# Optimization experiments

Hardware: AMD Instinct MI355X
Metric: run time of the kernel (lower is better)

Reference implementation:

```python
import jax, jax.numpy as jnp
import numpy as np

WS = 16          # window_size
NUM_HEADS = 6

def _rel_tables(ws):
    # SwinV2 continuous relative coords table, log-spaced, scaled by 8
    r = np.arange(-(ws - 1), ws, dtype=np.float32)
    t = np.stack(np.meshgrid(r, r, indexing='ij'), axis=-1)      # (2ws-1, 2ws-1, 2)
    t = t / (ws - 1) * 8.0
    t = np.sign(t) * np.log2(np.abs(t) + 1.0) / np.log2(8.0)
    c = np.stack(np.meshgrid(np.arange(ws), np.arange(ws), indexing='ij')).reshape(2, -1)
    rel = (c[:, :, None] - c[:, None, :]).transpose(1, 2, 0)     # (N, N, 2)
    rel[..., 0] += ws - 1
    rel[..., 1] += ws - 1
    rel[..., 0] *= 2 * ws - 1
    return jnp.asarray(t), jnp.asarray(rel.sum(-1))              # table, (N,N) int index

REL_TABLE, REL_INDEX = _rel_tables(WS)

def conv2d(x, w, b, pad=0, dil=1, groups=1):
    y = jax.lax.conv_general_dilated(
        x, w, (1, 1), [(pad, pad), (pad, pad)], rhs_dilation=(dil, dil),
        feature_group_count=groups, dimension_numbers=('NCHW', 'OIHW', 'NCHW'))
    return y + b[None, :, None, None]

def layernorm(x, g, b, eps=1e-5):
    mu = x.mean(-1, keepdims=True)
    var = ((x - mu) ** 2).mean(-1, keepdims=True)
    return (x - mu) * jax.lax.rsqrt(var + eps) * g + b

def _forward(x, p1_w, p1_b, pw_w, pw_b, dw_w, dw_b, dd_w, dd_b, p2_w, p2_b,
             ln_g, ln_b, qkv_w, q_bias, v_bias, logit_scale,
             cpb_w1, cpb_b1, cpb_w2, proj_w, proj_b):
    B, C, H, W = x.shape
    ws, nh = WS, NUM_HEADS
    N, hd = ws * ws, C // nh
    # ---- VAB: conv attention block ----
    y = jax.nn.gelu(conv2d(x, p1_w, p1_b), approximate=False)          # proj_1 + GELU
    a = conv2d(y, pw_w, pw_b)                                          # pointwise 1x1
    a = conv2d(a, dw_w, dw_b, pad=2, groups=C)                         # depthwise 5x5
    a = conv2d(a, dd_w, dd_b, pad=6, dil=3, groups=C)                  # depthwise 5x5 dil=3
    y = conv2d(y * a, p2_w, p2_b) + x                                  # proj_2 + residual
    y = jnp.transpose(y, (0, 2, 3, 1))                                 # B,H,W,C
    y = layernorm(y, ln_g, ln_b)                                       # pixel_norm
    # ---- window partition -> (B*nW, N, C) ----
    xw = y.reshape(B, H // ws, ws, W // ws, ws, C)
    xw = xw.transpose(0, 1, 3, 2, 4, 5).reshape(-1, N, C)
    # ---- SwinV2 cosine window attention ----
    qkv_b = jnp.concatenate([q_bias, jnp.zeros_like(v_bias), v_bias])
    qkv = (xw @ qkv_w.T + qkv_b).reshape(-1, N, 3, nh, hd).transpose(2, 0, 3, 1, 4)
    q, k, v = qkv[0], qkv[1], qkv[2]                                   # (B_, h, N, d)
    qn = q / jnp.maximum(jnp.linalg.norm(q, axis=-1, keepdims=True), 1e-12)
    kn = k / jnp.maximum(jnp.linalg.norm(k, axis=-1, keepdims=True), 1e-12)
    scale = jnp.exp(jnp.minimum(logit_scale, jnp.log(100.0)))          # clamp at 1/0.01
    attn = jnp.einsum('bhnd,bhmd->bhnm', qn, kn) * scale
    # CPB MLP bias: (2ws-1,2ws-1,2) -> heads, gathered by relative_position_index
    t = (jax.nn.relu(REL_TABLE @ cpb_w1.T + cpb_b1) @ cpb_w2.T).reshape(-1, nh)
    rpb = t[REL_INDEX.reshape(-1)].reshape(N, N, nh).transpose(2, 0, 1)
    attn = attn + 16.0 * jax.nn.sigmoid(rpb)
    attn = jax.nn.softmax(attn, axis=-1)
    out = jnp.einsum('bhnm,bhmd->bhnd', attn, v).transpose(0, 2, 1, 3).reshape(-1, N, C)
    out = out @ proj_w.T + proj_b
    # ---- window reverse -> NCHW ----
    out = out.reshape(B, H // ws, W // ws, ws, ws, C)
    out = out.transpose(0, 1, 3, 2, 4, 5).reshape(B, H, W, C)
    return jnp.transpose(out, (0, 3, 1, 2))

def setup_inputs():
    key = jax.random.key(0)
    ks = jax.random.split(key, 12)
    C, A = 192, 192
    rn = lambda k, shape, s=0.02: jax.random.normal(k, shape, jnp.float32) * s
    return {
        'x': jax.random.normal(ks[0], (4, C, 128, 128), jnp.float32),
        'p1_w': rn(ks[1], (A, C, 1, 1)), 'p1_b': jnp.zeros((A,), jnp.float32),
        'pw_w': rn(ks[2], (A, A, 1, 1)), 'pw_b': jnp.zeros((A,), jnp.float32),
        'dw_w': rn(ks[3], (A, 1, 5, 5), 0.05), 'dw_b': jnp.zeros((A,), jnp.float32),
        'dd_w': rn(ks[4], (A, 1, 5, 5), 0.05), 'dd_b': jnp.zeros((A,), jnp.float32),
        'p2_w': rn(ks[5], (C, A, 1, 1)), 'p2_b': jnp.zeros((C,), jnp.float32),
        'ln_g': jnp.ones((C,), jnp.float32), 'ln_b': jnp.zeros((C,), jnp.float32),
        'qkv_w': rn(ks[6], (3 * C, C)),
        'q_bias': jnp.zeros((C,), jnp.float32), 'v_bias': jnp.zeros((C,), jnp.float32),
        'logit_scale': jnp.log(10.0) * jnp.ones((NUM_HEADS, 1, 1), jnp.float32),
        'cpb_w1': rn(ks[7], (512, 2), 0.1), 'cpb_b1': jnp.zeros((512,), jnp.float32),
        'cpb_w2': rn(ks[8], (NUM_HEADS, 512), 0.1),
        'proj_w': rn(ks[9], (C, C)), 'proj_b': jnp.zeros((C,), jnp.float32),
    }

def reference(x, p1_w, p1_b, pw_w, pw_b, dw_w, dw_b, dd_w, dd_b, p2_w, p2_b,
              ln_g, ln_b, qkv_w, q_bias, v_bias, logit_scale,
              cpb_w1, cpb_b1, cpb_w2, proj_w, proj_b):
    return _forward(x, p1_w, p1_b, pw_w, pw_b, dw_w, dw_b, dd_w, dd_b, p2_w, p2_b,
                    ln_g, ln_b, qkv_w, q_bias, v_bias, logit_scale,
                    cpb_w1, cpb_b1, cpb_w2, proj_w, proj_b)
```

## Files before the change

### kernel.cpp

```cpp
#include <hip/hip_runtime.h>
#include <hip/hip_bf16.h>
#include <math.h>

#define HWC 16384
#define CCH 192
#define LDA 200

typedef __attribute__((ext_vector_type(8))) short short8x;
typedef __attribute__((ext_vector_type(4))) float f32x4;

__device__ __forceinline__ float b2f(unsigned int u){
  union { unsigned int i; float f; } x; x.i = (u & 0xffffu) << 16; return x.f;
}
__device__ __forceinline__ unsigned short f2b(float f){
  union { float f; unsigned int i; } x; x.f = f;
  unsigned int r = x.i + 0x7FFFu + ((x.i >> 16) & 1u);
  return (unsigned short)(r >> 16);
}
__device__ __forceinline__ unsigned int cvt_pk_bf16(float a, float b){
  unsigned int r;
  asm("v_cvt_pk_bf16_f32 %0, %1, %2" : "=v"(r) : "v"(a), "v"(b));
  return r;
}
__device__ __forceinline__ float exp2_fast(float x){
  float r;
  asm("v_exp_f32 %0, %1" : "=v"(r) : "v"(x));
  return r;
}
__device__ __forceinline__ float gelu_exact(float v){
  return 0.5f * v * (1.0f + erff(v * 0.70710678118654752440f));
}

__global__ __launch_bounds__(256) void cast_w_kernel(
    const float* __restrict__ qkvw, const float* __restrict__ projw,
    const float* __restrict__ p1w,  const float* __restrict__ pww,
    const float* __restrict__ p2w,  const float* __restrict__ dww,
    const float* __restrict__ ddw,
    unsigned short* __restrict__ wq,  unsigned short* __restrict__ wprj,
    unsigned short* __restrict__ wp1, unsigned short* __restrict__ wpa,
    unsigned short* __restrict__ wp2, float* __restrict__ dwt,
    float* __restrict__ ddt)
{
  int i = blockIdx.x*256 + threadIdx.x;
  if (i < 110592) wq[i] = f2b(qkvw[i]);
  if (i < 36864){
    wprj[i] = f2b(projw[i]);
    wp1[i]  = f2b(p1w[i]);
    wpa[i]  = f2b(pww[i]);
    wp2[i]  = f2b(p2w[i]);
  }
  if (i < 4992){
    int t = i / 192, c = i - t*192;
    dwt[i] = (t < 25) ? dww[c*25 + t] : 0.0f;
    ddt[i] = (t < 25) ? ddw[c*25 + t] : 0.0f;
  }
}

__global__ __launch_bounds__(256) void tx_kernel(
    const float* __restrict__ in, float* __restrict__ xt32,
    unsigned short* __restrict__ x16)
{
  __shared__ float xs[CCH*68];
  const int tid = threadIdx.x;
  const int pix0 = blockIdx.x * 64;
  const int bb = pix0 >> 14;
  const int hw0 = pix0 & (HWC-1);
  const long base = (long)bb * CCH * HWC + hw0;
  #pragma unroll 8
  for (int i=0;i<48;i++){
    int idx = tid + i*256;
    int ci = idx >> 6, pix = idx & 63;
    xs[ci*68 + pix] = in[base + (long)ci*HWC + pix];
  }
  __syncthreads();
  #pragma unroll 8
  for (int i=0;i<48;i++){
    int idx = tid + i*256;
    int pix = idx / 192, ci = idx - pix*192;
    float v = xs[ci*68 + pix];
    long g = (long)(pix0 + pix)*CCH + ci;
    xt32[g] = v;
    x16[g]  = f2b(v);
  }
}

__global__ __launch_bounds__(256, 3) void pw01_mfma(
    const unsigned short* __restrict__ x16,
    const unsigned short* __restrict__ w1,
    const float* __restrict__ b1,
    const unsigned short* __restrict__ wa,
    const float* __restrict__ ba,
    unsigned short* __restrict__ y16,
    unsigned short* __restrict__ a16)
{
  __shared__ unsigned short sA[128*LDA];
  const int tid = threadIdx.x;
  const int m0 = blockIdx.x * 128;
  #pragma unroll
  for (int i=0;i<12;i++){
    int idx = tid + i*256;
    int row = idx / 24, oct = idx - row*24;
    uint4 v = *(const uint4*)(x16 + (long)(m0+row)*CCH + oct*8);
    *(uint4*)&sA[row*LDA + oct*8] = v;
  }
  __syncthreads();
  const int wv = tid >> 6, lane = tid & 63;
  const int wm = (wv & 1) * 64;
  const int wn = (wv >> 1) * 96;
  const int l15 = lane & 15, q = lane >> 4;
  f32x4 acc[4][6];
  #pragma unroll
  for (int mi=0;mi<4;mi++)
    #pragma unroll
    for (int ni=0;ni<6;ni++) acc[mi][ni] = (f32x4){0.f,0.f,0.f,0.f};
  #pragma unroll
  for (int kk=0; kk<6; kk++){
    const int k0 = kk*32;
    short8x af[4], bf[6];
    #pragma unroll
    for (int mi=0; mi<4; mi++)
      af[mi] = *(const short8x*)&sA[(wm + mi*16 + l15)*LDA + k0 + q*8];
    #pragma unroll
    for (int ni=0; ni<6; ni++)
      bf[ni] = *(const short8x*)(w1 + (long)(wn + ni*16 + l15)*CCH + k0 + q*8);
    #pragma unroll
    for (int mi=0; mi<4; mi++)
      #pragma unroll
      for (int ni=0; ni<6; ni++)
        acc[mi][ni] = __builtin_amdgcn_mfma_f32_16x16x32_bf16(af[mi], bf[ni], acc[mi][ni], 0,0,0);
  }
  float bv[6];
  #pragma unroll
  for (int ni=0; ni<6; ni++) bv[ni] = b1[wn + ni*16 + l15];
  __syncthreads();
  #pragma unroll
  for (int mi=0; mi<4; mi++){
    #pragma unroll
    for (int r=0; r<4; r++){
      int pixl = wm + mi*16 + q*4 + r;
      long gp = (long)(m0 + pixl)*CCH + wn;
      #pragma unroll
      for (int ni=0; ni<6; ni++){
        unsigned short us = f2b(gelu_exact(acc[mi][ni][r] + bv[ni]));
        y16[gp + ni*16 + l15] = us;
        sA[pixl*LDA + wn + ni*16 + l15] = us;
      }
    }
  }
  __syncthreads();
  #pragma unroll
  for (int mi=0;mi<4;mi++)
    #pragma unroll
    for (int ni=0;ni<6;ni++) acc[mi][ni] = (f32x4){0.f,0.f,0.f,0.f};
  #pragma unroll
  for (int kk=0; kk<6; kk++){
    const int k0 = kk*32;
    short8x af[4], bf[6];
    #pragma unroll
    for (int mi=0; mi<4; mi++)
      af[mi] = *(const short8x*)&sA[(wm + mi*16 + l15)*LDA + k0 + q*8];
    #pragma unroll
    for (int ni=0; ni<6; ni++)
      bf[ni] = *(const short8x*)(wa + (long)(wn + ni*16 + l15)*CCH + k0 + q*8);
    #pragma unroll
    for (int mi=0; mi<4; mi++)
      #pragma unroll
      for (int ni=0; ni<6; ni++)
        acc[mi][ni] = __builtin_amdgcn_mfma_f32_16x16x32_bf16(af[mi], bf[ni], acc[mi][ni], 0,0,0);
  }
  #pragma unroll
  for (int ni=0; ni<6; ni++) bv[ni] = ba[wn + ni*16 + l15];
  #pragma unroll
  for (int mi=0; mi<4; mi++){
    #pragma unroll
    for (int r=0; r<4; r++){
      long gp = (long)(m0 + wm + mi*16 + q*4 + r)*CCH + wn;
      #pragma unroll
      for (int ni=0; ni<6; ni++)
        a16[gp + ni*16 + l15] = f2b(acc[mi][ni][r] + bv[ni]);
    }
  }
}

template<int MODE>
__global__ __launch_bounds__(256, 3) void pw_mfma(
    const unsigned short* __restrict__ in0,
    const unsigned short* __restrict__ in1,
    const unsigned short* __restrict__ w16,
    const float* __restrict__ bias,
    const float* __restrict__ xres,
    const float* __restrict__ gam, const float* __restrict__ bet,
    unsigned short* __restrict__ out16)
{
  __shared__ unsigned short sA[128*LDA];
  __shared__ float reds[128*2], reds2[128*2];
  const int tid = threadIdx.x;
  const int m0 = blockIdx.x * 128;
  #pragma unroll
  for (int i=0;i<12;i++){
    int idx = tid + i*256;
    int row = idx / 24, oct = idx - row*24;
    long g = (long)(m0+row)*CCH + oct*8;
    uint4 vy = *(const uint4*)(in0 + g);
    if (MODE == 2){
      uint4 va = *(const uint4*)(in1 + g);
      unsigned int yy[4] = {vy.x, vy.y, vy.z, vy.w};
      unsigned int aa[4] = {va.x, va.y, va.z, va.w};
      unsigned int rr[4];
      #pragma unroll
      for (int wq2=0; wq2<4; wq2++){
        float lo = b2f(yy[wq2]) * b2f(aa[wq2]);
        float hi = b2f(yy[wq2] >> 16) * b2f(aa[wq2] >> 16);
        rr[wq2] = (unsigned int)f2b(lo) | ((unsigned int)f2b(hi) << 16);
      }
      uint4 vp; vp.x=rr[0]; vp.y=rr[1]; vp.z=rr[2]; vp.w=rr[3];
      *(uint4*)&sA[row*LDA + oct*8] = vp;
    } else {
      *(uint4*)&sA[row*LDA + oct*8] = vy;
    }
  }
  __syncthreads();
  const int wv = tid >> 6, lane = tid & 63;
  const int wm = (wv & 1) * 64;
  const int wn = (wv >> 1) * 96;
  const int l15 = lane & 15, q = lane >> 4;
  f32x4 acc[4][6];
  #pragma unroll
  for (int mi=0;mi<4;mi++)
    #pragma unroll
    for (int ni=0;ni<6;ni++) acc[mi][ni] = (f32x4){0.f,0.f,0.f,0.f};
  #pragma unroll
  for (int kk=0; kk<6; kk++){
    const int k0 = kk*32;
    short8x af[4], bf[6];
    #pragma unroll
    for (int mi=0; mi<4; mi++)
      af[mi] = *(const short8x*)&sA[(wm + mi*16 + l15)*LDA + k0 + q*8];
    #pragma unroll
    for (int ni=0; ni<6; ni++)
      bf[ni] = *(const short8x*)(w16 + (long)(wn + ni*16 + l15)*CCH + k0 + q*8);
    #pragma unroll
    for (int mi=0; mi<4; mi++)
      #pragma unroll
      for (int ni=0; ni<6; ni++)
        acc[mi][ni] = __builtin_amdgcn_mfma_f32_16x16x32_bf16(af[mi], bf[ni], acc[mi][ni], 0,0,0);
  }
  float bv[6];
  #pragma unroll
  for (int ni=0; ni<6; ni++) bv[ni] = bias[wn + ni*16 + l15];

  if (MODE != 2){
    #pragma unroll
    for (int mi=0; mi<4; mi++){
      #pragma unroll
      for (int r=0; r<4; r++){
        long gp = (long)(m0 + wm + mi*16 + q*4 + r)*CCH + wn;
        #pragma unroll
        for (int ni=0; ni<6; ni++){
          float v = acc[mi][ni][r] + bv[ni];
          if (MODE == 0) v = gelu_exact(v);
          out16[gp + ni*16 + l15] = f2b(v);
        }
      }
    }
  } else {
    const int slot = wv >> 1;
    #pragma unroll
    for (int mi=0; mi<4; mi++){
      #pragma unroll
      for (int r=0; r<4; r++){
        int pixl = wm + mi*16 + q*4 + r;
        long gp = (long)(m0 + pixl)*CCH + wn;
        float s = 0.f, s2 = 0.f;
        #pragma unroll
        for (int ni=0; ni<6; ni++){
          float v = acc[mi][ni][r] + bv[ni] + xres[gp + ni*16 + l15];
          acc[mi][ni][r] = v;
          s += v; s2 = fmaf(v, v, s2);
        }
        s  += __shfl_xor(s, 1);  s  += __shfl_xor(s, 2);
        s  += __shfl_xor(s, 4);  s  += __shfl_xor(s, 8);
        s2 += __shfl_xor(s2, 1); s2 += __shfl_xor(s2, 2);
        s2 += __shfl_xor(s2, 4); s2 += __shfl_xor(s2, 8);
        if (l15 == 0){ reds[pixl*2 + slot] = s; reds2[pixl*2 + slot] = s2; }
      }
    }
    __syncthreads();
    #pragma unroll
    for (int mi=0; mi<4; mi++){
      #pragma unroll
      for (int r=0; r<4; r++){
        int pixl = wm + mi*16 + q*4 + r;
        long gp = (long)(m0 + pixl)*CCH + wn;
        float st  = reds[pixl*2] + reds[pixl*2+1];
        float s2t = reds2[pixl*2] + reds2[pixl*2+1];
        float mu = st * (1.0f/192.0f);
        float var = s2t * (1.0f/192.0f) - mu*mu;
        float rs = rsqrtf(var + 1e-5f);
        #pragma unroll
        for (int ni=0; ni<6; ni++){
          int co = wn + ni*16 + l15;
          float z = (acc[mi][ni][r] - mu) * rs * gam[co] + bet[co];
          out16[gp + ni*16 + l15] = f2b(z);
        }
      }
    }
  }
}

template<int PAD, int DIL>
__global__ __launch_bounds__(256) void dw_nhwc(
    const unsigned short* __restrict__ in16, const float* __restrict__ wT,
    const float* __restrict__ bias, unsigned short* __restrict__ out16)
{
  const int g = blockIdx.x;
  const int wid = (g & 7) * 768 + (g >> 3);
  const int t = wid*256 + threadIdx.x;
  const int c8 = t % 24, pix = t / 24;
  const int row = (pix >> 7) & 127, col = pix & 127;
  const int c0 = c8 * 8;
  const long ibase = (long)(pix & ~(HWC-1)) * CCH;
  const unsigned short* pbase = in16 + ibase + c0;

  uint4 xv[25];
  #pragma unroll
  for (int kh=0; kh<5; kh++){
    int ihc = min(max(row + kh*DIL - PAD, 0), 127);
    #pragma unroll
    for (int kw=0; kw<5; kw++){
      int iwc = min(max(col + kw*DIL - PAD, 0), 127);
      xv[kh*5+kw] = *(const uint4*)(pbase + (long)(ihc*128 + iwc)*CCH);
    }
  }
  float acc[8];
  {
    float4 b0 = *(const float4*)&bias[c0], b1 = *(const float4*)&bias[c0+4];
    acc[0]=b0.x; acc[1]=b0.y; acc[2]=b0.z; acc[3]=b0.w;
    acc[4]=b1.x; acc[5]=b1.y; acc[6]=b1.z; acc[7]=b1.w;
  }
  #pragma unroll
  for (int kh=0; kh<5; kh++){
    bool vh = (unsigned)(row + kh*DIL - PAD) < 128u;
    #pragma unroll
    for (int kw=0; kw<5; kw++){
      bool v = vh && ((unsigned)(col + kw*DIL - PAD) < 128u);
      const float* wp = wT + (v ? (kh*5 + kw) : 25)*CCH + c0;
      float4 w0 = *(const float4*)wp, w1 = *(const float4*)(wp + 4);
      uint4 xq = xv[kh*5+kw];
      unsigned int uu[4] = {xq.x, xq.y, xq.z, xq.w};
      float wa[8] = {w0.x, w0.y, w0.z, w0.w, w1.x, w1.y, w1.z, w1.w};
      #pragma unroll
      for (int j=0; j<8; j++){
        float xvf = b2f(uu[j>>1] >> ((j&1)*16));
        acc[j] = fmaf(wa[j], xvf, acc[j]);
      }
    }
  }
  unsigned int rr[4];
  #pragma unroll
  for (int wq2=0; wq2<4; wq2++)
    rr[wq2] = (unsigned int)f2b(acc[wq2*2]) | ((unsigned int)f2b(acc[wq2*2+1]) << 16);
  uint4 o; o.x=rr[0]; o.y=rr[1]; o.z=rr[2]; o.w=rr[3];
  *(uint4*)(out16 + (long)pix*CCH + c0) = o;
}

__global__ __launch_bounds__(256, 3) void qkv_fused(
    const unsigned short* __restrict__ z16,
    const unsigned short* __restrict__ w16,
    const float* __restrict__ qb, const float* __restrict__ vb,
    unsigned short* __restrict__ qkvb)
{
  __shared__ unsigned short sA[128*LDA];
  const int tid = threadIdx.x;
  const int m0 = blockIdx.x * 128;
  #pragma unroll
  for (int i=0;i<12;i++){
    int idx = tid + i*256;
    int row = idx / 24, oct = idx - row*24;
    uint4 v = *(const uint4*)(z16 + (long)(m0+row)*CCH + oct*8);
    *(uint4*)&sA[row*LDA + oct*8] = v;
  }
  __syncthreads();
  const int wv = tid >> 6, lane = tid & 63;
  const int wm = (wv & 1) * 64;
  const int wn = (wv >> 1) * 96;
  const int l15 = lane & 15, q = lane >> 4;
  const int head0 = wn >> 5;
  int winm[4], tokb[4];
  #pragma unroll
  for (int mi=0;mi<4;mi++){
    int pb = m0 + wm + mi*16;
    int hw = pb & (HWC-1);
    int row = hw >> 7, col = hw & 127;
    winm[mi] = (pb>>14)*64 + (row>>4)*8 + (col>>4);
    tokb[mi] = (row & 15) * 16;
  }
  #pragma unroll
  for (int s=0; s<3; s++){
    const unsigned short* wbase = w16 + (long)(s*192)*CCH;
    f32x4 acc[4][6];
    #pragma unroll
    for (int mi=0;mi<4;mi++)
      #pragma unroll
      for (int ni=0;ni<6;ni++) acc[mi][ni] = (f32x4){0.f,0.f,0.f,0.f};
    #pragma unroll
    for (int kk=0; kk<6; kk++){
      const int k0 = kk*32;
      short8x af[4], bf[6];
      #pragma unroll
      for (int mi=0; mi<4; mi++)
        af[mi] = *(const short8x*)&sA[(wm + mi*16 + l15)*LDA + k0 + q*8];
      #pragma unroll
      for (int ni=0; ni<6; ni++)
        bf[ni] = *(const short8x*)(wbase + (long)(wn + ni*16 + l15)*CCH + k0 + q*8);
      #pragma unroll
      for (int mi=0; mi<4; mi++)
        #pragma unroll
        for (int ni=0; ni<6; ni++)
          acc[mi][ni] = __builtin_amdgcn_mfma_f32_16x16x32_bf16(af[mi], bf[ni], acc[mi][ni], 0,0,0);
    }
    float bvv[6];
    #pragma unroll
    for (int ni=0;ni<6;ni++){
      int co = wn + ni*16 + l15;
      bvv[ni] = (s==0) ? qb[co] : ((s==2) ? vb[co] : 0.0f);
    }
    unsigned short* dst = qkvb + (long)s * 12582912;
    #pragma unroll
    for (int mi=0; mi<4; mi++){
      long obase = (long)winm[mi]*49152 + (long)tokb[mi]*32 + l15*2;
      #pragma unroll
      for (int r=0; r<4; r++){
        long ob = obase + (q*4 + r)*32;
        #pragma unroll
        for (int hp=0; hp<3; hp++){
          unsigned int u = (unsigned int)f2b(acc[mi][hp*2][r]   + bvv[hp*2])
                         | ((unsigned int)f2b(acc[mi][hp*2+1][r] + bvv[hp*2+1]) << 16);
          *(unsigned int*)&dst[ob + (long)(head0 + hp)*8192] = u;
        }
      }
    }
  }
}

__device__ __forceinline__ float cpb_coord(int a){
  float r = ((float)a - 15.0f) * (8.0f/15.0f);
  float t = log2f(fabsf(r) + 1.0f) * (1.0f/3.0f);
  return (r < 0.f) ? -t : t;
}
__global__ __launch_bounds__(128) void cpb_mlp_kernel(
    const float* __restrict__ w1, const float* __restrict__ b1,
    const float* __restrict__ w2, float* __restrict__ tbl6)
{
  int e = blockIdx.x;
  int a = e / 31, bb = e - a*31;
  float t0 = cpb_coord(a), t1 = cpb_coord(bb);
  float p[6] = {0,0,0,0,0,0};
  for (int hh = threadIdx.x; hh < 512; hh += 128){
    float hid = t0*w1[hh*2] + t1*w1[hh*2+1] + b1[hh];
    hid = fmaxf(hid, 0.0f);
    #pragma unroll
    for (int hd=0; hd<6; hd++) p[hd] = fmaf(hid, w2[hd*512 + hh], p[hd]);
  }
  __shared__ float red[6][128];
  #pragma unroll
  for (int hd=0; hd<6; hd++) red[hd][threadIdx.x] = p[hd];
  __syncthreads();
  if (threadIdx.x < 6){
    float sum = 0.f;
    for (int i=0;i<128;i++) sum += red[threadIdx.x][i];
    tbl6[e*6 + threadIdx.x] = sum;
  }
}
__global__ __launch_bounds__(256) void cpb_expand_kernel(
    const float* __restrict__ tbl6, float* __restrict__ bias)
{
  int idx = blockIdx.x*256 + threadIdx.x;
  int h = idx >> 16;
  int rem = idx & 65535;
  int i = rem >> 8, j = rem & 255;
  int dy = (i>>4) - (j>>4) + 15;
  int dx = (i&15) - (j&15) + 15;
  float v = tbl6[(dy*31+dx)*6 + h];
  bias[idx] = (16.0f / (1.0f + __expf(-v)) - 16.0f) * 1.4426950408889634f;
}

#define KSP 40
#define VTP 264
__global__ __launch_bounds__(256) void attn_mfma(
    const unsigned short* __restrict__ qkvb, const float* __restrict__ bias,
    const float* __restrict__ ls,
    unsigned short* __restrict__ aout)
{
  __shared__ unsigned short ks[256*KSP];
  __shared__ unsigned short vt[32*VTP];
  __shared__ unsigned short ps[4][64*KSP];
  __shared__ float qinvs[256];
  const int win = blockIdx.x, h = blockIdx.y;
  const int t = threadIdx.x;
  const long base = ((long)(win*6 + h)) << 13;
  const unsigned short* Qg = qkvb + base;
  const unsigned short* Kg = Qg + 12582912;
  const unsigned short* Vg = Kg + 12582912;
  const float sc = __expf(fminf(ls[h], 4.60517018598809136804f));

  {
    union { uint4 v4[4]; unsigned int u[16]; } kb, ko, qv;
    const unsigned short* kr = Kg + t*32;
    #pragma unroll
    for (int o=0;o<4;o++) kb.v4[o] = *(const uint4*)(kr + o*8);
    float sk = 0.f;
    #pragma unroll
    for (int i=0;i<16;i++){
      float lo = b2f(kb.u[i]), hi = b2f(kb.u[i]>>16);
      sk = fmaf(lo, lo, sk); sk = fmaf(hi, hi, sk);
    }
    float kinv = 1.0f / fmaxf(sqrtf(sk), 1e-12f);
    #pragma unroll
    for (int i=0;i<16;i++)
      ko.u[i] = cvt_pk_bf16(b2f(kb.u[i])*kinv, b2f(kb.u[i]>>16)*kinv);
    #pragma unroll
    for (int o=0;o<4;o++) *(uint4*)&ks[t*KSP + o*8] = ko.v4[o];

    const unsigned short* qr = Qg + t*32;
    #pragma unroll
    for (int o=0;o<4;o++) qv.v4[o] = *(const uint4*)(qr + o*8);
    float sq = 0.f;
    #pragma unroll
    for (int i=0;i<16;i++){
      float lo = b2f(qv.u[i]), hi = b2f(qv.u[i]>>16);
      sq = fmaf(lo, lo, sq); sq = fmaf(hi, hi, sq);
    }
    qinvs[t] = sc * 1.4426950408889634f / fmaxf(sqrtf(sq), 1e-12f);
  }
  {
    const int kt = t >> 5, j = t & 31;
    const int col = kt*32 + ((j & 15)*2 + (j >> 4));
    union { unsigned short u[32]; uint4 v4[4]; } vp;
    const unsigned short* vr = Vg + t*32;
    #pragma unroll
    for (int o=0;o<4;o++) vp.v4[o] = *(const uint4*)(vr + o*8);
    #pragma unroll
    for (int d=0; d<32; d++) vt[d*VTP + col] = vp.u[d];
  }
  const int wv = t >> 6, lane = t & 63;
  const int l15 = lane & 15, q = lane >> 4;
  short8x qa[4];
  #pragma unroll
  for (int mi=0; mi<4; mi++)
    qa[mi] = *(const short8x*)(Qg + (wv*64 + mi*16 + l15)*32 + q*8);
  __syncthreads();

  float4 qiv[4];
  #pragma unroll
  for (int mi=0; mi<4; mi++)
    qiv[mi] = *(const float4*)&qinvs[wv*64 + mi*16 + q*4];

  f32x4 oacc[4][2], lsum[4];
  #pragma unroll
  for (int mi=0;mi<4;mi++){
    oacc[mi][0] = (f32x4){0.f,0.f,0.f,0.f};
    oacc[mi][1] = (f32x4){0.f,0.f,0.f,0.f};
    lsum[mi]    = (f32x4){0.f,0.f,0.f,0.f};
  }
  const float* bias_h = bias + (h << 16);
  unsigned short* myps = ps[wv];

  for (int kt=0; kt<8; kt++){
    const int k0 = kt*32;
    short8x kb0 = *(const short8x*)&ks[(k0 + l15)*KSP + q*8];
    short8x kb1 = *(const short8x*)&ks[(k0 + 16 + l15)*KSP + q*8];
    f32x4 s[4][2];
    __builtin_amdgcn_s_setprio(1);
    #pragma unroll
    for (int mi=0; mi<4; mi++){
      f32x4 z0 = (f32x4){0.f,0.f,0.f,0.f};
      s[mi][0] = __builtin_amdgcn_mfma_f32_16x16x32_bf16(qa[mi], kb0, z0, 0,0,0);
      s[mi][1] = __builtin_amdgcn_mfma_f32_16x16x32_bf16(qa[mi], kb1, z0, 0,0,0);
    }
    __builtin_amdgcn_s_setprio(0);
    #pragma unroll
    for (int mi=0; mi<4; mi++){
      const float* qivp = (const float*)&qiv[mi];
      #pragma unroll
      for (int r=0; r<4; r++){
        int rowq = wv*64 + mi*16 + q*4 + r;
        const float* brow = bias_h + rowq*256 + k0;
        float qr2 = qivp[r];
        float e0 = exp2_fast(fminf(fmaf(s[mi][0][r], qr2, brow[l15]),      43.f));
        float e1 = exp2_fast(fminf(fmaf(s[mi][1][r], qr2, brow[16 + l15]), 43.f));
        lsum[mi][r] += e0 + e1;
        *(unsigned int*)&myps[(mi*16 + q*4 + r)*KSP + l15*2] = cvt_pk_bf16(e0, e1);
      }
    }
    short8x vb0 = *(const short8x*)&vt[(l15)*VTP      + k0 + q*8];
    short8x vb1 = *(const short8x*)&vt[(16 + l15)*VTP + k0 + q*8];
    __builtin_amdgcn_s_setprio(1);
    #pragma unroll
    for (int mi=0; mi<4; mi++){
      short8x pa = *(const short8x*)&myps[(mi*16 + l15)*KSP + q*8];
      oacc[mi][0] = __builtin_amdgcn_mfma_f32_16x16x32_bf16(pa, vb0, oacc[mi][0], 0,0,0);
      oacc[mi][1] = __builtin_amdgcn_mfma_f32_16x16x32_bf16(pa, vb1, oacc[mi][1], 0,0,0);
    }
    __builtin_amdgcn_s_setprio(0);
  }
  #pragma unroll
  for (int mi=0; mi<4; mi++){
    #pragma unroll
    for (int r=0; r<4; r++){
      float v = lsum[mi][r];
      v += __shfl_xor(v, 1);
      v += __shfl_xor(v, 2);
      v += __shfl_xor(v, 4);
      v += __shfl_xor(v, 8);
      lsum[mi][r] = v;
    }
  }
  const int dperm = (l15 >> 1) + ((l15 & 1) << 4);
  const int bb = win >> 6, wy = (win >> 3) & 7, wx = win & 7;
  #pragma unroll
  for (int mi=0; mi<4; mi++){
    #pragma unroll
    for (int r=0; r<4; r++){
      int rowq = wv*64 + mi*16 + q*4 + r;
      int pixo = bb*HWC + (wy*16 + (rowq>>4))*128 + wx*16 + (rowq&15);
      float inv = 1.0f / lsum[mi][r];
      aout[(long)pixo*CCH + h*32 + dperm]     = f2b(oacc[mi][0][r]*inv);
      aout[(long)pixo*CCH + h*32 + dperm + 8] = f2b(oacc[mi][1][r]*inv);
    }
  }
}

__global__ __launch_bounds__(256, 3) void proj_mfma(
    const unsigned short* __restrict__ a16,
    const unsigned short* __restrict__ w16,
    const float* __restrict__ bias,
    float* __restrict__ outp)
{
  __shared__ unsigned short sB[128*LDA];
  const int tid = threadIdx.x;
  const int n0 = blockIdx.x * 128;
  #pragma unroll
  for (int i=0;i<12;i++){
    int idx = tid + i*256;
    int row = idx / 24, oct = idx - row*24;
    uint4 v = *(const uint4*)(a16 + (long)(n0+row)*CCH + oct*8);
    *(uint4*)&sB[row*LDA + oct*8] = v;
  }
  __syncthreads();
  const int wv = tid >> 6, lane = tid & 63;
  const int wm = (wv & 1) * 96;
  const int wn = (wv >> 1) * 64;
  const int l15 = lane & 15, q = lane >> 4;
  f32x4 acc[6][4];
  #pragma unroll
  for (int mi=0;mi<6;mi++)
    #pragma unroll
    for (int ni=0;ni<4;ni++) acc[mi][ni] = (f32x4){0.f,0.f,0.f,0.f};
  #pragma unroll
  for (int kk=0; kk<6; kk++){
    const int k0 = kk*32;
    short8x af[6], bf[4];
    #pragma unroll
    for (int mi=0; mi<6; mi++)
      af[mi] = *(const short8x*)(w16 + (long)(wm + mi*16 + l15)*CCH + k0 + q*8);
    #pragma unroll
    for (int ni=0; ni<4; ni++)
      bf[ni] = *(const short8x*)&sB[(wn + ni*16 + l15)*LDA + k0 + q*8];
    #pragma unroll
    for (int mi=0; mi<6; mi++)
      #pragma unroll
      for (int ni=0; ni<4; ni++)
        acc[mi][ni] = __builtin_amdgcn_mfma_f32_16x16x32_bf16(af[mi], bf[ni], acc[mi][ni], 0,0,0);
  }
  #pragma unroll
  for (int mi=0; mi<6; mi++){
    #pragma unroll
    for (int r=0; r<4; r++){
      int co = wm + mi*16 + q*4 + r;
      float bv = bias[co];
      #pragma unroll
      for (int ni=0; ni<4; ni++){
        int pix = n0 + wn + ni*16 + l15;
        int b = pix >> 14, hw = pix & (HWC-1);
        outp[((long)b*CCH + co)*HWC + hw] = acc[mi][ni][r] + bv;
      }
    }
  }
}

extern "C" void kernel_launch(void* const* d_in, const int* in_sizes, int n_in,
                              void* d_out, int out_size, void* d_ws, size_t ws_size,
                              hipStream_t stream)
{
  const float* x       = (const float*)d_in[0];
  const float* p1_w    = (const float*)d_in[1];
  const float* p1_b    = (const float*)d_in[2];
  const float* pw_w    = (const float*)d_in[3];
  const float* pw_b    = (const float*)d_in[4];
  const float* dw_w    = (const float*)d_in[5];
  const float* dw_b    = (const float*)d_in[6];
  const float* dd_w    = (const float*)d_in[7];
  const float* dd_b    = (const float*)d_in[8];
  const float* p2_w    = (const float*)d_in[9];
  const float* p2_b    = (const float*)d_in[10];
  const float* ln_g    = (const float*)d_in[11];
  const float* ln_b    = (const float*)d_in[12];
  const float* qkv_w   = (const float*)d_in[13];
  const float* q_bias  = (const float*)d_in[14];
  const float* v_bias  = (const float*)d_in[15];
  const float* lscale  = (const float*)d_in[16];
  const float* cpb_w1  = (const float*)d_in[17];
  const float* cpb_b1  = (const float*)d_in[18];
  const float* cpb_w2  = (const float*)d_in[19];
  const float* proj_w  = (const float*)d_in[20];
  const float* proj_b  = (const float*)d_in[21];

  float* ws = (float*)d_ws;
  const long A = 12582912L;
  unsigned short* X16  = (unsigned short*)ws;
  unsigned short* Y16  = (unsigned short*)(ws + A/2);
  unsigned short* A16  = (unsigned short*)(ws + A);
  unsigned short* T16  = (unsigned short*)(ws + A + A/2);
  float* XT32 = ws + 2*A;
  unsigned short* QKVB = (unsigned short*)ws;
  unsigned short* Z16  = (unsigned short*)(ws + 3*A);
  unsigned short* AO16 = Z16;
  float* DWT = ws + 3*A + A/2;
  float* DDT = DWT + 4992;
  unsigned short* WQ   = (unsigned short*)(DDT + 4992);
  unsigned short* WPRJ = WQ + 110592;
  unsigned short* WP1  = WPRJ + 36864;
  unsigned short* WPA  = WP1 + 36864;
  unsigned short* WP2  = WPA + 36864;
  float* RB = ws + 4*A;
  float* T6 = RB + 393216;

  cast_w_kernel<<<432, 256, 0, stream>>>(qkv_w, proj_w, p1_w, pw_w, p2_w, dw_w, dd_w,
                                         WQ, WPRJ, WP1, WPA, WP2, DWT, DDT);
  cpb_mlp_kernel<<<961, 128, 0, stream>>>(cpb_w1, cpb_b1, cpb_w2, T6);
  cpb_expand_kernel<<<1536, 256, 0, stream>>>(T6, RB);

  tx_kernel<<<1024, 256, 0, stream>>>(x, XT32, X16);

  pw01_mfma<<<512, 256, 0, stream>>>(X16, WP1, p1_b, WPA, pw_b, Y16, A16);
  dw_nhwc<2,1><<<6144, 256, 0, stream>>>(A16, DWT, dw_b, T16);
  dw_nhwc<6,3><<<6144, 256, 0, stream>>>(T16, DDT, dd_b, A16);
  pw_mfma<2><<<512, 256, 0, stream>>>(Y16, A16, WP2, p2_b, XT32, ln_g, ln_b, Z16);

  qkv_fused<<<512, 256, 0, stream>>>(Z16, WQ, q_bias, v_bias, QKVB);

  attn_mfma<<<dim3(256, 6), 256, 0, stream>>>(QKVB, RB, lscale, AO16);

  proj_mfma<<<512, 256, 0, stream>>>(AO16, WPRJ, proj_b, (float*)d_out);
}
```

Measured before the change: 483.1 us.

## Tile depthwise convs through shared memory with halo staging per 32x32 block

```diff
diff --git a/kernel.cpp b/kernel.cpp
--- a/kernel.cpp
+++ b/kernel.cpp
@@ -309,59 +309,67 @@
 }
 
 template<int PAD, int DIL>
-__global__ __launch_bounds__(256) void dw_nhwc(
+__global__ __launch_bounds__(256) void dw_tile(
     const unsigned short* __restrict__ in16, const float* __restrict__ wT,
     const float* __restrict__ bias, unsigned short* __restrict__ out16)
 {
-  const int g = blockIdx.x;
-  const int wid = (g & 7) * 768 + (g >> 3);
-  const int t = wid*256 + threadIdx.x;
-  const int c8 = t % 24, pix = t / 24;
-  const int row = (pix >> 7) & 127, col = pix & 127;
-  const int c0 = c8 * 8;
-  const long ibase = (long)(pix & ~(HWC-1)) * CCH;
-  const unsigned short* pbase = in16 + ibase + c0;
-
-  uint4 xv[25];
-  #pragma unroll
-  for (int kh=0; kh<5; kh++){
-    int ihc = min(max(row + kh*DIL - PAD, 0), 127);
-    #pragma unroll
-    for (int kw=0; kw<5; kw++){
-      int iwc = min(max(col + kw*DIL - PAD, 0), 127);
-      xv[kh*5+kw] = *(const uint4*)(pbase + (long)(ihc*128 + iwc)*CCH);
-    }
-  }
-  float acc[8];
-  {
-    float4 b0 = *(const float4*)&bias[c0], b1 = *(const float4*)&bias[c0+4];
-    acc[0]=b0.x; acc[1]=b0.y; acc[2]=b0.z; acc[3]=b0.w;
-    acc[4]=b1.x; acc[5]=b1.y; acc[6]=b1.z; acc[7]=b1.w;
-  }
-  #pragma unroll
-  for (int kh=0; kh<5; kh++){
-    bool vh = (unsigned)(row + kh*DIL - PAD) < 128u;
-    #pragma unroll
-    for (int kw=0; kw<5; kw++){
-      bool v = vh && ((unsigned)(col + kw*DIL - PAD) < 128u);
-      const float* wp = wT + (v ? (kh*5 + kw) : 25)*CCH + c0;
-      float4 w0 = *(const float4*)wp, w1 = *(const float4*)(wp + 4);
-      uint4 xq = xv[kh*5+kw];
-      unsigned int uu[4] = {xq.x, xq.y, xq.z, xq.w};
-      float wa[8] = {w0.x, w0.y, w0.z, w0.w, w1.x, w1.y, w1.z, w1.w};
-      #pragma unroll
-      for (int j=0; j<8; j++){
-        float xvf = b2f(uu[j>>1] >> ((j&1)*16));
-        acc[j] = fmaf(wa[j], xvf, acc[j]);
-      }
-    }
-  }
-  unsigned int rr[4];
-  #pragma unroll
-  for (int wq2=0; wq2<4; wq2++)
-    rr[wq2] = (unsigned int)f2b(acc[wq2*2]) | ((unsigned int)f2b(acc[wq2*2+1]) << 16);
-  uint4 o; o.x=rr[0]; o.y=rr[1]; o.z=rr[2]; o.w=rr[3];
-  *(uint4*)(out16 + (long)pix*CCH + c0) = o;
+  constexpr int R = 32 + 2*PAD;
+  constexpr int NPX = R*R;
+  constexpr int NIT = (NPX + 255) / 256;
+  __shared__ unsigned short sIn[NPX*8];
+  const int bid = blockIdx.x;
+  const int t_lo = bid & 7, rest = bid >> 3;
+  const int c8 = rest % 24, t_hi = rest / 24;
+  const int tile = t_lo + 8*t_hi;
+  const int b = tile >> 4, ty = (tile >> 2) & 3, tx = tile & 3;
+  const int c0 = c8*8;
+  const int tid = threadIdx.x;
+  const long ibase = (long)b * HWC * CCH;
+  const int r0 = ty*32 - PAD, cl0 = tx*32 - PAD;
+  #pragma unroll
+  for (int j=0; j<NIT; j++){
+    int idx = tid + j*256;
+    if (idx < NPX){
+      int r = idx / R, c = idx - r*R;
+      int gr = min(max(r0 + r, 0), 127), gc = min(max(cl0 + c, 0), 127);
+      *(uint4*)&sIn[idx*8] = *(const uint4*)(in16 + ibase + (long)(gr*128 + gc)*CCH + c0);
+    }
+  }
+  __syncthreads();
+  const float4 bb0 = *(const float4*)&bias[c0], bb1 = *(const float4*)&bias[c0+4];
+  #pragma unroll
+  for (int it=0; it<4; it++){
+    int o = tid + it*256;
+    int orow = o >> 5, ocol = o & 31;
+    float acc[8] = {bb0.x, bb0.y, bb0.z, bb0.w, bb1.x, bb1.y, bb1.z, bb1.w};
+    #pragma unroll
+    for (int kh=0; kh<5; kh++){
+      bool vh = (unsigned)(ty*32 + orow + kh*DIL - PAD) < 128u;
+      int lr = orow + kh*DIL;
+      #pragma unroll
+      for (int kw=0; kw<5; kw++){
+        bool v = vh && ((unsigned)(tx*32 + ocol + kw*DIL - PAD) < 128u);
+        int lc = ocol + kw*DIL;
+        uint4 xq = *(const uint4*)&sIn[(lr*R + lc)*8];
+        const float* wp = wT + (v ? (kh*5 + kw) : 25)*CCH + c0;
+        float4 w0 = *(const float4*)wp, w1 = *(const float4*)(wp + 4);
+        unsigned int uu[4] = {xq.x, xq.y, xq.z, xq.w};
+        float wa[8] = {w0.x, w0.y, w0.z, w0.w, w1.x, w1.y, w1.z, w1.w};
+        #pragma unroll
+        for (int jj=0; jj<8; jj++){
+          float xvf = b2f(uu[jj>>1] >> ((jj&1)*16));
+          acc[jj] = fmaf(wa[jj], xvf, acc[jj]);
+        }
+      }
+    }
+    int gr = ty*32 + orow, gc = tx*32 + ocol;
+    unsigned int rr[4];
+    #pragma unroll
+    for (int wq2=0; wq2<4; wq2++)
+      rr[wq2] = (unsigned int)f2b(acc[wq2*2]) | ((unsigned int)f2b(acc[wq2*2+1]) << 16);
+    uint4 ov; ov.x=rr[0]; ov.y=rr[1]; ov.z=rr[2]; ov.w=rr[3];
+    *(uint4*)(out16 + ibase + (long)(gr*128 + gc)*CCH + c0) = ov;
+  }
 }
 
 __global__ __launch_bounds__(256, 3) void qkv_fused(
@@ -744,8 +752,8 @@
   tx_kernel<<<1024, 256, 0, stream>>>(x, XT32, X16);
 
   pw01_mfma<<<512, 256, 0, stream>>>(X16, WP1, p1_b, WPA, pw_b, Y16, A16);
-  dw_nhwc<2,1><<<6144, 256, 0, stream>>>(A16, DWT, dw_b, T16);
-  dw_nhwc<6,3><<<6144, 256, 0, stream>>>(T16, DDT, dd_b, A16);
+  dw_tile<2,1><<<1536, 256, 0, stream>>>(A16, DWT, dw_b, T16);
+  dw_tile<6,3><<<1536, 256, 0, stream>>>(T16, DDT, dd_b, A16);
   pw_mfma<2><<<512, 256, 0, stream>>>(Y16, A16, WP2, p2_b, XT32, ln_g, ln_b, Z16);
 
   qkv_fused<<<512, 256, 0, stream>>>(Z16, WQ, q_bias, v_bias, QKVB);
```

Measured after the change: 470.3 us. 2.7% less time.
